# Performance work log

Measured on AMD Instinct MI355X. Metric: run time of the kernel, lower is better.

Reference implementation:

```python
import jax, jax.numpy as jnp
import numpy as np

B, N, D, H = 256, 128, 512, 512

def setup_inputs() -> dict:
    key = jax.random.key(0)
    k1, k2, k3, k4 = jax.random.split(key, 4)
    X = jax.random.normal(k1, (B, N, D), dtype=jnp.float32)
    A = jax.random.uniform(k2, (B, N, N), dtype=jnp.float32)
    # fc: Linear(D, H) params, kaiming-uniform-ish init
    lim = 1.0 / np.sqrt(D)
    W = jax.random.uniform(k3, (H, D), minval=-lim, maxval=lim, dtype=jnp.float32)
    b = jax.random.uniform(k4, (H,), minval=-lim, maxval=lim, dtype=jnp.float32)
    ln_w = jnp.ones((H,), dtype=jnp.float32)
    ln_b = jnp.zeros((H,), dtype=jnp.float32)
    return {"X": X, "A": A, "W": W, "b": b, "ln_w": ln_w, "ln_b": ln_b}

def reference(X, A, W, b, ln_w, ln_b):
    # row-normalize adjacency: A / (sum_j A[b,i,j] + 1e-6)
    A_norm = A / (jnp.sum(A, axis=2, keepdims=True) + 1e-6)
    # aggregate neighbors: (B,N,N) @ (B,N,D) -> (B,N,D)
    X_neighbor = jnp.einsum('bnm,bmd->bnd', A_norm, X)
    X_agg = X + X_neighbor
    # linear D -> H
    X_up = jnp.einsum('bnd,hd->bnh', X_agg, W) + b
    # layernorm over last dim (eps=1e-5 matches torch default)
    mu = jnp.mean(X_up, axis=-1, keepdims=True)
    var = jnp.mean(jnp.square(X_up - mu), axis=-1, keepdims=True)
    X_ln = (X_up - mu) / jnp.sqrt(var + 1e-5) * ln_w + ln_b
    return jax.nn.sigmoid(X_ln)
```

## Files before the change

### kernel.cpp

```cpp
#include <hip/hip_runtime.h>
#include <cstdint>

#define BB 256
#define NN 128
#define DD 512
#define HH 512

typedef __attribute__((ext_vector_type(8))) short bf16x8;
typedef __attribute__((ext_vector_type(16))) float f32x16;
typedef unsigned short u16;

static __device__ __forceinline__ u16 f2bf(float f) {
    union { float f; uint32_t u; } v; v.f = f;
    uint32_t u = v.u;
    return (u16)((u + 0x7FFFu + ((u >> 16) & 1u)) >> 16);
}

static __device__ __forceinline__ void gload16(const u16* g, u16* l) {
    __builtin_amdgcn_global_load_lds((const __attribute__((address_space(1))) void*)g,
                                     (__attribute__((address_space(3))) void*)l, 16, 0, 0);
}

__global__ __launch_bounds__(256) void wconv_kernel(const float* __restrict__ W, u16* __restrict__ Wb) {
    int idx = (blockIdx.x * 256 + threadIdx.x) * 4;
    float4 v = *(const float4*)(W + idx);
    ushort4 o;
    o.x = f2bf(v.x); o.y = f2bf(v.y); o.z = f2bf(v.z); o.w = f2bf(v.w);
    *(ushort4*)(Wb + idx) = o;
}

__global__ __launch_bounds__(512, 1) void fused_kernel(const float* __restrict__ X, const float* __restrict__ A,
                                                       const u16* __restrict__ Wb, const float* __restrict__ bias,
                                                       const float* __restrict__ lnw, const float* __restrict__ lnb,
                                                       float* __restrict__ out) {
    __shared__ __align__(16) char smem[163840];
    u16* Ms = (u16*)smem;
    u16* Xt = (u16*)(smem + 32768);
    float* Pss = (float*)smem;
    float* musig = (float*)(smem + 4096);

    const int t = threadIdx.x;
    const int lane = t & 63, w = t >> 6, l31 = lane & 31, lh = lane >> 5;
    const int batch = blockIdx.x;
    const int wm = w >> 2, wn = w & 3;

    {
        const int row = t >> 2, seg = t & 3;
        const float* Ag = A + (size_t)batch * NN * NN + row * NN + seg * 32;
        float4 a[8];
        #pragma unroll
        for (int j = 0; j < 8; ++j) a[j] = *(const float4*)(Ag + j * 4);
        float s = 0.f;
        #pragma unroll
        for (int j = 0; j < 8; ++j) s += a[j].x + a[j].y + a[j].z + a[j].w;
        s += __shfl_xor(s, 1);
        s += __shfl_xor(s, 2);
        const float inv = 1.0f / (s + 1e-6f);
        #pragma unroll
        for (int c2 = 0; c2 < 4; ++c2) {
            u16 tmp[8];
            const float* pe = (const float*)&a[c2 * 2];
            #pragma unroll
            for (int e = 0; e < 8; ++e) {
                int m = seg * 32 + c2 * 8 + e;
                tmp[e] = f2bf(pe[e] * inv + (m == row ? 1.0f : 0.0f));
            }
            int c = seg * 4 + c2;
            *(uint4*)(Ms + row * 128 + ((c ^ (row & 15)) << 3)) = *(const uint4*)tmp;
        }
    }

    {
        const float* Xg = X + (size_t)batch * NN * DD;
        #pragma unroll
        for (int it = 0; it < 32; ++it) {
            int q = it * 512 + t;
            int m = q >> 7, c4 = q & 127;
            float4 v = *(const float4*)(Xg + (size_t)m * DD + c4 * 4);
            float fv[4] = {v.x, v.y, v.z, v.w};
            #pragma unroll
            for (int j = 0; j < 4; ++j) {
                int d = c4 * 4 + j;
                Xt[d * 128 + (((m >> 3) ^ ((d >> 2) & 7)) << 3) + (m & 7)] = f2bf(fv[j]);
            }
        }
    }
    __syncthreads();

    #pragma unroll
    for (int dh = 0; dh < 2; ++dh) {
        f32x16 acc1[2][2];
        #pragma unroll
        for (int fi = 0; fi < 2; ++fi)
            #pragma unroll
            for (int fd = 0; fd < 2; ++fd)
                #pragma unroll
                for (int r = 0; r < 16; ++r)
                    acc1[fi][fd][r] = 0.f;

        #pragma unroll
        for (int ksl = 0; ksl < 8; ++ksl) {
            const int kc = ksl * 2 + lh;
            bf16x8 af[2], bx[2];
            #pragma unroll
            for (int fi = 0; fi < 2; ++fi) {
                int i = wm * 64 + fi * 32 + l31;
                af[fi] = *(const bf16x8*)(Ms + i * 128 + ((kc ^ (i & 15)) << 3));
            }
            #pragma unroll
            for (int fd = 0; fd < 2; ++fd) {
                int d = dh * 256 + wn * 64 + fd * 32 + l31;
                bx[fd] = *(const bf16x8*)(Xt + d * 128 + ((kc ^ ((d >> 2) & 7)) << 3));
            }
            #pragma unroll
            for (int fi = 0; fi < 2; ++fi)
                #pragma unroll
                for (int fd = 0; fd < 2; ++fd)
                    acc1[fi][fd] = __builtin_amdgcn_mfma_f32_32x32x16_bf16(af[fi], bx[fd], acc1[fi][fd], 0, 0, 0);
        }
        __syncthreads();

        char* Xa = smem + 32768 + dh * 65536;
        #pragma unroll
        for (int fi = 0; fi < 2; ++fi)
            #pragma unroll
            for (int r = 0; r < 16; ++r) {
                int i = wm * 64 + fi * 32 + (r & 3) + 8 * (r >> 2) + 4 * lh;
                #pragma unroll
                for (int fd = 0; fd < 2; ++fd) {
                    int dl = wn * 64 + fd * 32 + l31;
                    *(u16*)(Xa + i * 512 + (((dl >> 3) ^ (i & 7)) << 4) + (dl & 7) * 2) = f2bf(acc1[fi][fd][r]);
                }
            }
        __syncthreads();
    }

    float bias_v[2][2], lnw_v[2][2], lnb_v[2][2];
    #pragma unroll
    for (int ch = 0; ch < 2; ++ch)
        #pragma unroll
        for (int fh = 0; fh < 2; ++fh) {
            int h = ch * 256 + wn * 64 + fh * 32 + l31;
            bias_v[ch][fh] = bias[h];
            lnw_v[ch][fh] = lnw[h];
            lnb_v[ch][fh] = lnb[h];
        }

    f32x16 acc[2][2][2];
    #pragma unroll
    for (int ch = 0; ch < 2; ++ch)
        #pragma unroll
        for (int fi = 0; fi < 2; ++fi)
            #pragma unroll
            for (int fh = 0; fh < 2; ++fh)
                #pragma unroll
                for (int r = 0; r < 16; ++r)
                    acc[ch][fi][fh][r] = 0.f;

#define STAGEW(CH, KS, BUF)                                                               \
    {                                                                                     \
        u16* dst_ = (u16*)(smem + (BUF) * 16384);                                         \
        _Pragma("unroll")                                                                 \
        for (int it_ = 0; it_ < 2; ++it_) {                                               \
            int q_ = it_ * 512 + t;                                                       \
            int h_ = q_ >> 2, cc_ = q_ & 3;                                               \
            gload16(Wb + (size_t)((CH) * 256 + h_) * DD + (KS) * 32 +                     \
                        ((cc_ ^ ((h_ >> 1) & 3)) * 8),                                    \
                    dst_ + q_ * 8);                                                       \
        }                                                                                 \
    }

#define GEMM2_PASS(CH)                                                                    \
    {                                                                                     \
        STAGEW(CH, 0, 0);                                                                 \
        __syncthreads();                                                                  \
        for (int ks = 0; ks < 16; ++ks) {                                                 \
            const int buf = ks & 1;                                                       \
            if (ks < 15) STAGEW(CH, ks + 1, buf ^ 1);                                     \
            const u16* wl = (const u16*)(smem + buf * 16384);                             \
            _Pragma("unroll")                                                             \
            for (int s2 = 0; s2 < 2; ++s2) {                                              \
                const int kc = s2 * 2 + lh;                                               \
                const int ccg = ks * 4 + kc;                                              \
                const int xdh = ccg >> 5, cloc = ccg & 31;                                \
                const char* Xa = smem + 32768 + xdh * 65536;                              \
                bf16x8 af[2], bw[2];                                                      \
                _Pragma("unroll")                                                         \
                for (int fi = 0; fi < 2; ++fi) {                                          \
                    int m = wm * 64 + fi * 32 + l31;                                      \
                    af[fi] = *(const bf16x8*)(Xa + m * 512 + ((cloc ^ (m & 7)) << 4));    \
                }                                                                         \
                _Pragma("unroll")                                                         \
                for (int fh = 0; fh < 2; ++fh) {                                          \
                    int hl = wn * 64 + fh * 32 + l31;                                     \
                    bw[fh] = *(const bf16x8*)(wl + hl * 32 + ((kc ^ ((hl >> 1) & 3)) * 8)); \
                }                                                                         \
                _Pragma("unroll")                                                         \
                for (int fi = 0; fi < 2; ++fi)                                            \
                    _Pragma("unroll")                                                     \
                    for (int fh = 0; fh < 2; ++fh)                                        \
                        acc[CH][fi][fh] = __builtin_amdgcn_mfma_f32_32x32x16_bf16(        \
                            af[fi], bw[fh], acc[CH][fi][fh], 0, 0, 0);                    \
            }                                                                             \
            __syncthreads();                                                              \
        }                                                                                 \
    }

    GEMM2_PASS(0);
    GEMM2_PASS(1);
#undef STAGEW
#undef GEMM2_PASS

    float rs[2][16], rss[2][16];
    #pragma unroll
    for (int fi = 0; fi < 2; ++fi)
        #pragma unroll
        for (int r = 0; r < 16; ++r) {
            float s = 0.f, ss = 0.f;
            #pragma unroll
            for (int ch = 0; ch < 2; ++ch)
                #pragma unroll
                for (int fh = 0; fh < 2; ++fh) {
                    float a = acc[ch][fi][fh][r] + bias_v[ch][fh];
                    acc[ch][fi][fh][r] = a;
                    s += a; ss += a * a;
                }
            rs[fi][r] = s; rss[fi][r] = ss;
        }
    #pragma unroll
    for (int msk = 1; msk <= 16; msk <<= 1) {
        #pragma unroll
        for (int fi = 0; fi < 2; ++fi)
            #pragma unroll
            for (int r = 0; r < 16; ++r) {
                rs[fi][r] += __shfl_xor(rs[fi][r], msk);
                rss[fi][r] += __shfl_xor(rss[fi][r], msk);
            }
    }
    if (l31 == 0) {
        #pragma unroll
        for (int fi = 0; fi < 2; ++fi)
            #pragma unroll
            for (int r = 0; r < 16; ++r) {
                int row = wm * 64 + fi * 32 + (r & 3) + 8 * (r >> 2) + 4 * lh;
                float2 v; v.x = rs[fi][r]; v.y = rss[fi][r];
                *(float2*)(Pss + (wn * 128 + row) * 2) = v;
            }
    }
    __syncthreads();
    if (t < 128) {
        float s = 0.f, ss = 0.f;
        #pragma unroll
        for (int q = 0; q < 4; ++q) {
            float2 v = *(const float2*)(Pss + (q * 128 + t) * 2);
            s += v.x; ss += v.y;
        }
        float mean = s * (1.0f / 512.0f);
        float var = ss * (1.0f / 512.0f) - mean * mean;
        float2 mz; mz.x = mean; mz.y = rsqrtf(var + 1e-5f);
        *(float2*)(musig + t * 2) = mz;
    }
    __syncthreads();

    float* Og = out + (size_t)batch * NN * HH;
    #pragma unroll
    for (int fi = 0; fi < 2; ++fi)
        #pragma unroll
        for (int r = 0; r < 16; ++r) {
            int row = wm * 64 + fi * 32 + (r & 3) + 8 * (r >> 2) + 4 * lh;
            float2 mz = *(const float2*)(musig + row * 2);
            #pragma unroll
            for (int ch = 0; ch < 2; ++ch)
                #pragma unroll
                for (int fh = 0; fh < 2; ++fh) {
                    float xn = (acc[ch][fi][fh][r] - mz.x) * mz.y * lnw_v[ch][fh] + lnb_v[ch][fh];
                    Og[(size_t)row * HH + ch * 256 + wn * 64 + fh * 32 + l31] =
                        1.0f / (1.0f + __expf(-xn));
                }
        }
}

extern "C" void kernel_launch(void* const* d_in, const int* in_sizes, int n_in,
                              void* d_out, int out_size, void* d_ws, size_t ws_size,
                              hipStream_t stream) {
    const float* X = (const float*)d_in[0];
    const float* A = (const float*)d_in[1];
    const float* W = (const float*)d_in[2];
    const float* bias = (const float*)d_in[3];
    const float* lnw = (const float*)d_in[4];
    const float* lnb = (const float*)d_in[5];
    float* out = (float*)d_out;

    u16* Wb = (u16*)d_ws;

    hipLaunchKernelGGL(wconv_kernel, dim3(256), dim3(256), 0, stream, W, Wb);
    hipLaunchKernelGGL(fused_kernel, dim3(256), dim3(512), 0, stream, X, A, Wb, bias, lnw, lnb, out);
}
```

Before: 87.59 us.

## Split second GEMM and layernorm epilogue into two row halves to cut accumulators

The W-projection GEMM plus the layernorm/sigmoid epilogue now runs twice, once per 64-row half of the 128 nodes. This halves the live MFMA accumulators per thread (4 tiles instead of 8), which lowers register pressure and may avoid spills or allow better scheduling. The cost is that the bf16 W matrix is streamed from global into LDS twice per block, and each half adds its own barriers and reduction steps.

```diff
diff --git a/kernel.cpp b/kernel.cpp
--- a/kernel.cpp
+++ b/kernel.cpp
@@ -145,17 +145,7 @@
             lnw_v[ch][fh] = lnw[h];
             lnb_v[ch][fh] = lnb[h];
         }
-
-    f32x16 acc[2][2][2];
-    #pragma unroll
-    for (int ch = 0; ch < 2; ++ch)
-        #pragma unroll
-        for (int fi = 0; fi < 2; ++fi)
-            #pragma unroll
-            for (int fh = 0; fh < 2; ++fh)
-                #pragma unroll
-                for (int r = 0; r < 16; ++r)
-                    acc[ch][fi][fh][r] = 0.f;
+    float* Og = out + (size_t)batch * NN * HH;
 
 #define STAGEW(CH, KS, BUF)                                                               \
     {                                                                                     \
@@ -170,8 +160,9 @@
         }                                                                                 \
     }
 
-#define GEMM2_PASS(CH)                                                                    \
+#define GEMM2_PASS(RH, CH)                                                                \
     {                                                                                     \
+        __syncthreads();              \
         STAGEW(CH, 0, 0);                                                                 \
         __syncthreads();                                                                  \
         for (int ks = 0; ks < 16; ++ks) {                                                 \
@@ -184,100 +175,99 @@
                 const int ccg = ks * 4 + kc;                                              \
                 const int xdh = ccg >> 5, cloc = ccg & 31;                                \
                 const char* Xa = smem + 32768 + xdh * 65536;                              \
-                bf16x8 af[2], bw[2];                                                      \
-                _Pragma("unroll")                                                         \
-                for (int fi = 0; fi < 2; ++fi) {                                          \
-                    int m = wm * 64 + fi * 32 + l31;                                      \
-                    af[fi] = *(const bf16x8*)(Xa + m * 512 + ((cloc ^ (m & 7)) << 4));    \
-                }                                                                         \
+                const int i_ = (RH) * 64 + wm * 32 + l31;                                 \
+                bf16x8 af = *(const bf16x8*)(Xa + i_ * 512 + ((cloc ^ (i_ & 7)) << 4));   \
+                bf16x8 bw[2];                                                             \
                 _Pragma("unroll")                                                         \
                 for (int fh = 0; fh < 2; ++fh) {                                          \
                     int hl = wn * 64 + fh * 32 + l31;                                     \
                     bw[fh] = *(const bf16x8*)(wl + hl * 32 + ((kc ^ ((hl >> 1) & 3)) * 8)); \
                 }                                                                         \
                 _Pragma("unroll")                                                         \
-                for (int fi = 0; fi < 2; ++fi)                                            \
-                    _Pragma("unroll")                                                     \
-                    for (int fh = 0; fh < 2; ++fh)                                        \
-                        acc[CH][fi][fh] = __builtin_amdgcn_mfma_f32_32x32x16_bf16(        \
-                            af[fi], bw[fh], acc[CH][fi][fh], 0, 0, 0);                    \
+                for (int fh = 0; fh < 2; ++fh)                                            \
+                    acc2[CH][fh] = __builtin_amdgcn_mfma_f32_32x32x16_bf16(               \
+                        af, bw[fh], acc2[CH][fh], 0, 0, 0);                               \
             }                                                                             \
             __syncthreads();                                                              \
         }                                                                                 \
     }
 
-    GEMM2_PASS(0);
-    GEMM2_PASS(1);
+#define ROWHALF(RH)                                                                       \
+    {                                                                                     \
+        f32x16 acc2[2][2];                                                                \
+        _Pragma("unroll")                                                                 \
+        for (int ch = 0; ch < 2; ++ch)                                                    \
+            _Pragma("unroll")                                                             \
+            for (int fh = 0; fh < 2; ++fh)                                                \
+                _Pragma("unroll")                                                         \
+                for (int r = 0; r < 16; ++r)                                              \
+                    acc2[ch][fh][r] = 0.f;                                                \
+        GEMM2_PASS(RH, 0);                                                                \
+        GEMM2_PASS(RH, 1);                                                                \
+                       \
+        float rs[16], rss[16];                                                            \
+        _Pragma("unroll")                                                                 \
+        for (int r = 0; r < 16; ++r) {                                                    \
+            float s = 0.f, ss = 0.f;                                                      \
+            _Pragma("unroll")                                                             \
+            for (int ch = 0; ch < 2; ++ch)                                                \
+                _Pragma("unroll")                                                         \
+                for (int fh = 0; fh < 2; ++fh) {                                          \
+                    float a = acc2[ch][fh][r] + bias_v[ch][fh];                           \
+                    acc2[ch][fh][r] = a;                                                  \
+                    s += a; ss += a * a;                                                  \
+                }                                                                         \
+            rs[r] = s; rss[r] = ss;                                                       \
+        }                                                                                 \
+        _Pragma("unroll")                                                                 \
+        for (int msk = 1; msk <= 16; msk <<= 1)                                           \
+            _Pragma("unroll")                                                             \
+            for (int r = 0; r < 16; ++r) {                                                \
+                rs[r] += __shfl_xor(rs[r], msk);                                          \
+                rss[r] += __shfl_xor(rss[r], msk);                                        \
+            }                                                                             \
+        if (l31 == 0) {                                                                   \
+            _Pragma("unroll")                                                             \
+            for (int r = 0; r < 16; ++r) {                                                \
+                int rl = wm * 32 + (r & 3) + 8 * (r >> 2) + 4 * lh;                       \
+                float2 v; v.x = rs[r]; v.y = rss[r];                                      \
+                *(float2*)(Pss + (wn * 64 + rl) * 2) = v;                                 \
+            }                                                                             \
+        }                                                                                 \
+        __syncthreads();                                                                  \
+        if (t < 64) {                                                                     \
+            float s = 0.f, ss = 0.f;                                                      \
+            _Pragma("unroll")                                                             \
+            for (int q = 0; q < 4; ++q) {                                                 \
+                float2 v = *(const float2*)(Pss + (q * 64 + t) * 2);                      \
+                s += v.x; ss += v.y;                                                      \
+            }                                                                             \
+            float mean = s * (1.0f / 512.0f);                                             \
+            float var = ss * (1.0f / 512.0f) - mean * mean;                               \
+            float2 mz; mz.x = mean; mz.y = rsqrtf(var + 1e-5f);                           \
+            *(float2*)(musig + t * 2) = mz;                                               \
+        }                                                                                 \
+        __syncthreads();                                                                  \
+        _Pragma("unroll")                                                                 \
+        for (int r = 0; r < 16; ++r) {                                                    \
+            int rl = wm * 32 + (r & 3) + 8 * (r >> 2) + 4 * lh;                           \
+            float2 mz = *(const float2*)(musig + rl * 2);                                 \
+            _Pragma("unroll")                                                             \
+            for (int ch = 0; ch < 2; ++ch)                                                \
+                _Pragma("unroll")                                                         \
+                for (int fh = 0; fh < 2; ++fh) {                                          \
+                    float xn = (acc2[ch][fh][r] - mz.x) * mz.y * lnw_v[ch][fh] + lnb_v[ch][fh]; \
+                    Og[(size_t)((RH) * 64 + rl) * HH + ch * 256 + wn * 64 + fh * 32 + l31] =    \
+                        1.0f / (1.0f + __expf(-xn));                                      \
+                }                                                                         \
+        }                                                                                 \
+    }
+
+    ROWHALF(0);
+    ROWHALF(1);
 #undef STAGEW
 #undef GEMM2_PASS
-
-    float rs[2][16], rss[2][16];
-    #pragma unroll
-    for (int fi = 0; fi < 2; ++fi)
-        #pragma unroll
-        for (int r = 0; r < 16; ++r) {
-            float s = 0.f, ss = 0.f;
-            #pragma unroll
-            for (int ch = 0; ch < 2; ++ch)
-                #pragma unroll
-                for (int fh = 0; fh < 2; ++fh) {
-                    float a = acc[ch][fi][fh][r] + bias_v[ch][fh];
-                    acc[ch][fi][fh][r] = a;
-                    s += a; ss += a * a;
-                }
-            rs[fi][r] = s; rss[fi][r] = ss;
-        }
-    #pragma unroll
-    for (int msk = 1; msk <= 16; msk <<= 1) {
-        #pragma unroll
-        for (int fi = 0; fi < 2; ++fi)
-            #pragma unroll
-            for (int r = 0; r < 16; ++r) {
-                rs[fi][r] += __shfl_xor(rs[fi][r], msk);
-                rss[fi][r] += __shfl_xor(rss[fi][r], msk);
-            }
-    }
-    if (l31 == 0) {
-        #pragma unroll
-        for (int fi = 0; fi < 2; ++fi)
-            #pragma unroll
-            for (int r = 0; r < 16; ++r) {
-                int row = wm * 64 + fi * 32 + (r & 3) + 8 * (r >> 2) + 4 * lh;
-                float2 v; v.x = rs[fi][r]; v.y = rss[fi][r];
-                *(float2*)(Pss + (wn * 128 + row) * 2) = v;
-            }
-    }
-    __syncthreads();
-    if (t < 128) {
-        float s = 0.f, ss = 0.f;
-        #pragma unroll
-        for (int q = 0; q < 4; ++q) {
-            float2 v = *(const float2*)(Pss + (q * 128 + t) * 2);
-            s += v.x; ss += v.y;
-        }
-        float mean = s * (1.0f / 512.0f);
-        float var = ss * (1.0f / 512.0f) - mean * mean;
-        float2 mz; mz.x = mean; mz.y = rsqrtf(var + 1e-5f);
-        *(float2*)(musig + t * 2) = mz;
-    }
-    __syncthreads();
-
-    float* Og = out + (size_t)batch * NN * HH;
-    #pragma unroll
-    for (int fi = 0; fi < 2; ++fi)
-        #pragma unroll
-        for (int r = 0; r < 16; ++r) {
-            int row = wm * 64 + fi * 32 + (r & 3) + 8 * (r >> 2) + 4 * lh;
-            float2 mz = *(const float2*)(musig + row * 2);
-            #pragma unroll
-            for (int ch = 0; ch < 2; ++ch)
-                #pragma unroll
-                for (int fh = 0; fh < 2; ++fh) {
-                    float xn = (acc[ch][fi][fh][r] - mz.x) * mz.y * lnw_v[ch][fh] + lnb_v[ch][fh];
-                    Og[(size_t)row * HH + ch * 256 + wn * 64 + fh * 32 + l31] =
-                        1.0f / (1.0f + __expf(-xn));
-                }
-        }
+#undef ROWHALF
 }
 
 extern "C" void kernel_launch(void* const* d_in, const int* in_sizes, int n_in,
```

Result: no change. 87.69 us (+0.1%).
